# Performance work log

Hardware: AMD Instinct MI355X
Metric: run time of the kernel (lower is better)

Reference implementation:

```python
import jax, jax.numpy as jnp
import numpy as np

R = 2        # pixel-shuffle upscale
CN = 32      # channel_nums
COL = 3      # colors
NM = 6       # module_nums (2 convs each -> 12 backbone convs)
QMAX_A = 255.0   # uint8 activation fake-quant range
QMAX_W = 127.0   # int8 (narrow) weight fake-quant range


def fq_act(x, s):
    # Brevitas Uint8ActPerTensorFloat fake-quant with STE
    v = x / s
    q = jnp.clip(jnp.round(v), 0.0, QMAX_A)
    return s * (v + jax.lax.stop_gradient(q - v))


def fq_w(w, s):
    # Int8WeightPerTensorFloat (symmetric, narrow range) fake-quant with STE
    v = w / s
    q = jnp.clip(jnp.round(v), -QMAX_W, QMAX_W)
    return s * (v + jax.lax.stop_gradient(q - v))


def conv3(x, w, b):
    y = jax.lax.conv_general_dilated(
        x, w, window_strides=(1, 1), padding=((1, 1), (1, 1)),
        dimension_numbers=("NCHW", "OIHW", "NCHW"))
    return y + b[None, :, None, None]


def qblock(x, w, b, sw, act_s):
    # QuantConv3X3: quant_in -> quant conv (+bias) -> QuantReLU (relu + quant)
    xq = fq_act(x, act_s)
    y = conv3(xq, fq_w(w, sw), b)
    y = jax.nn.relu(y)
    return fq_act(y, act_s)


def pixel_shuffle(x, r):
    B, C, H, W = x.shape
    c = C // (r * r)
    x = x.reshape(B, c, r, r, H, W)
    x = x.transpose(0, 1, 4, 2, 5, 3)   # B, c, H, r, W, r
    return x.reshape(B, c, H * r, W * r)


def _forward(x, head_w, head_b, head_sw, bb_w, bb_b, bb_sw, tr_w, tr_b, tr_sw, act_s):
    y0 = qblock(x, head_w, head_b, head_sw, act_s)

    def step(y, p):
        w, b, sw = p
        return qblock(y, w, b, sw, act_s), None

    y, _ = jax.lax.scan(step, y0, (bb_w, bb_b, bb_sw))
    y = qblock(y + y0, tr_w, tr_b, tr_sw, act_s)   # act_type='linear' still hits QuantReLU branch
    y = jnp.clip(y, 0.0, 255.0)
    return pixel_shuffle(y, R)


def setup_inputs() -> dict:
    key = jax.random.key(0)
    ks = jax.random.split(key, 4)
    B, H, W = 8, 256, 256
    x = jax.random.uniform(ks[0], (B, COL, H, W), dtype=jnp.float32) * 255.0
    head_w = jax.random.normal(ks[1], (CN, COL, 3, 3), dtype=jnp.float32) * 0.05
    head_b = jnp.zeros((CN,), jnp.float32)
    bb_w = jax.random.normal(ks[2], (2 * NM, CN, CN, 3, 3), dtype=jnp.float32) * 0.05
    bb_b = jnp.zeros((2 * NM, CN), jnp.float32)
    tr_w = jax.random.normal(ks[3], (COL * R * R, CN, 3, 3), dtype=jnp.float32) * 0.05
    tr_b = jnp.zeros((COL * R * R,), jnp.float32)
    head_sw = jnp.max(jnp.abs(head_w)) / QMAX_W
    bb_sw = jnp.max(jnp.abs(bb_w), axis=(1, 2, 3, 4)) / QMAX_W
    tr_sw = jnp.max(jnp.abs(tr_w)) / QMAX_W
    act_s = jnp.float32(1.0)
    return dict(x=x, head_w=head_w, head_b=head_b, head_sw=head_sw,
                bb_w=bb_w, bb_b=bb_b, bb_sw=bb_sw,
                tr_w=tr_w, tr_b=tr_b, tr_sw=tr_sw, act_s=act_s)


def reference(x, head_w, head_b, head_sw, bb_w, bb_b, bb_sw, tr_w, tr_b, tr_sw, act_s):
    return _forward(x, head_w, head_b, head_sw, bb_w, bb_b, bb_sw, tr_w, tr_b, tr_sw, act_s)
```

## Files before the change

### kernel.cpp

```cpp
#include <hip/hip_runtime.h>

typedef __bf16 bf16x8 __attribute__((ext_vector_type(8)));
typedef float  f32x16 __attribute__((ext_vector_type(16)));

__global__ __launch_bounds__(256) void quantw_kernel(
    const float* __restrict__ src, float* __restrict__ dst,
    const float* __restrict__ sw, int per_layer_sw, int OC, int ICK, int total)
{
    int i = blockIdx.x * 256 + threadIdx.x;
    if (i >= total) return;
    int per = OC * ICK;
    int l = i / per;
    int rem = i - l * per;
    int oc = rem / ICK;
    int k = rem - oc * ICK;
    float s = sw[per_layer_sw ? l : 0];
    float v = rintf(src[i] / s);
    v = fminf(fmaxf(v, -127.0f), 127.0f);
    dst[l * per + k * OC + oc] = v;
}

__global__ __launch_bounds__(256) void packb_kernel(
    const float* __restrict__ src, unsigned short* __restrict__ dst,
    const float* __restrict__ sw, int per_layer_sw, int OC_real, int total)
{
    int i = blockIdx.x * 256 + threadIdx.x;
    if (i >= total) return;
    int l   = i / 9216;
    int r   = i - l * 9216;
    int s   = r >> 9;
    int lane = (r >> 3) & 63;
    int j   = r & 7;
    int k   = s * 16 + ((lane >> 5) << 3) + j;
    int tap = k >> 5;
    int ic  = k & 31;
    int oc  = lane & 31;
    unsigned short v = 0;
    if (oc < OC_real) {
        float scale = sw[per_layer_sw ? l : 0];
        float w = src[((l * OC_real + oc) * 32 + ic) * 9 + tap];
        float q = rintf(w / scale);
        q = fminf(fmaxf(q, -127.0f), 127.0f);
        union { float f; unsigned int u; } cv; cv.f = q;
        v = (unsigned short)(cv.u >> 16);
    }
    dst[i] = v;
}

__global__ __launch_bounds__(256) void head_kernel(
    const float* __restrict__ x, const float* __restrict__ wq,
    const float* __restrict__ bias, const float* __restrict__ sw_ptr,
    const float* __restrict__ s_ptr, unsigned char* __restrict__ out)
{
    __shared__ unsigned char tile[3][10][34];
    const int tid = threadIdx.x;
    const int x0 = blockIdx.x * 32;
    const int y0 = blockIdx.y * 8;
    const int b  = blockIdx.z;
    const float s = s_ptr[0];

    for (int ch = 0; ch < 3; ++ch) {
        const int base = (b * 3 + ch) << 16;
        for (int p = tid; p < 10 * 34; p += 256) {
            int r = p / 34, c = p - r * 34;
            int gy = y0 + r - 1, gx = x0 + c - 1;
            unsigned char v = 0;
            if ((unsigned)gy < 256u && (unsigned)gx < 256u) {
                float xv = x[base + (gy << 8) + gx];
                float q = (s == 1.0f) ? xv : (xv / s);
                q = rintf(q);
                q = fminf(fmaxf(q, 0.0f), 255.0f);
                v = (unsigned char)q;
            }
            tile[ch][r][c] = v;
        }
    }
    __syncthreads();

    const int c = tid & 31, r = tid >> 5;
    float acc[32];
    #pragma unroll
    for (int i = 0; i < 32; ++i) acc[i] = 0.0f;

    #pragma unroll
    for (int ic = 0; ic < 3; ++ic) {
        float a[9];
        #pragma unroll
        for (int dy = 0; dy < 3; ++dy)
            #pragma unroll
            for (int dx = 0; dx < 3; ++dx)
                a[dy * 3 + dx] = (float)tile[ic][r + dy][c + dx];
        #pragma unroll
        for (int t = 0; t < 9; ++t) {
            const float* wrow = wq + (ic * 9 + t) * 32;
            #pragma unroll
            for (int oc = 0; oc < 32; ++oc)
                acc[oc] = fmaf(a[t], wrow[oc], acc[oc]);
        }
    }

    const float alpha = s * sw_ptr[0];
    unsigned int w8[8] = {0,0,0,0,0,0,0,0};
    #pragma unroll
    for (int oc = 0; oc < 32; ++oc) {
        float y = fmaf(alpha, acc[oc], bias[oc]);
        y = fmaxf(y, 0.0f);
        float v = (s == 1.0f) ? y : (y / s);
        v = rintf(v);
        v = fminf(fmaxf(v, 0.0f), 255.0f);
        w8[oc >> 2] |= ((unsigned int)(unsigned char)v) << (8 * (oc & 3));
    }
    uint4* dst = (uint4*)(out + (size_t)((((b << 8) + (y0 + r)) << 8) + (x0 + c)) * 32);
    dst[0] = make_uint4(w8[0], w8[1], w8[2], w8[3]);
    dst[1] = make_uint4(w8[4], w8[5], w8[6], w8[7]);
}

template<bool FINAL>
__global__ __launch_bounds__(256, 2) void qconv_mfma_kernel(
    const unsigned char* __restrict__ in,
    const unsigned char* __restrict__ resid,
    const unsigned short* __restrict__ Bp,
    const float* __restrict__ bias,
    const float* __restrict__ sw_ptr, int sw_idx,
    const float* __restrict__ s_ptr,
    void* __restrict__ out)
{
    __shared__ uint4 aT[2448];
    __shared__ uint4 bT[1152];
    const int tid = threadIdx.x;
    const int x0 = blockIdx.x << 5;
    const int y0 = blockIdx.y << 4;
    const int b  = blockIdx.z;

    #pragma unroll
    for (int it = 0; it < 5; ++it) {
        int bi = tid + it * 256;
        if (bi < 1152) bT[bi] = ((const uint4*)Bp)[bi];
    }
    #pragma unroll
    for (int it = 0; it < 5; ++it) {
        int ci = tid + it * 256;
        if (ci < 1224) {
            int yt  = ci / 68;
            int rem = ci - yt * 68;
            int xt  = rem >> 1;
            int ch  = rem & 1;
            int gy = y0 + yt - 1;
            int gx = x0 + xt - 1;
            uint4 raw = make_uint4(0, 0, 0, 0);
            uint4 res = make_uint4(0, 0, 0, 0);
            if ((unsigned)gy < 256u && (unsigned)gx < 256u) {
                size_t off = (size_t)((((b << 8) + gy) << 8) + gx) * 32 + (ch << 4);
                raw = *(const uint4*)(in + off);
                if (FINAL) res = *(const uint4*)(resid + off);
            }
            unsigned int ow[8];
            const unsigned int* rw = (const unsigned int*)&raw;
            const unsigned int* rr = (const unsigned int*)&res;
            #pragma unroll
            for (int w = 0; w < 4; ++w) {
                unsigned int v = rw[w], rv = rr[w];
                #pragma unroll
                for (int hb = 0; hb < 2; ++hb) {
                    unsigned int a0 = (v >> (16 * hb)) & 0xffu;
                    unsigned int a1 = (v >> (16 * hb + 8)) & 0xffu;
                    if (FINAL) {
                        a0 += (rv >> (16 * hb)) & 0xffu;      if (a0 > 255u) a0 = 255u;
                        a1 += (rv >> (16 * hb + 8)) & 0xffu;  if (a1 > 255u) a1 = 255u;
                    }
                    union { float f; unsigned int u; } c0, c1;
                    c0.f = (float)a0; c1.f = (float)a1;
                    ow[2 * w + hb] = (c0.u >> 16) | (c1.u & 0xffff0000u);
                }
            }
            int swz  = (xt & 3) ^ ((xt >> 2) & 3);
            int base = (yt * 34 + xt) << 2;
            aT[base + (((ch << 1) + 0) ^ swz)] = make_uint4(ow[0], ow[1], ow[2], ow[3]);
            aT[base + (((ch << 1) + 1) ^ swz)] = make_uint4(ow[4], ow[5], ow[6], ow[7]);
        }
    }
    __syncthreads();

    const int lane = tid & 63;
    const int wid  = tid >> 6;
    const int px   = lane & 31;
    const int half = lane >> 5;
    const int py0  = wid << 2;

    f32x16 acc[4];
    #pragma unroll
    for (int p = 0; p < 4; ++p)
        #pragma unroll
        for (int i = 0; i < 16; ++i) acc[p][i] = 0.0f;

    #pragma unroll
    for (int ich = 0; ich < 2; ++ich) {
        bf16x8 af[6][3];
        #pragma unroll
        for (int yl = 0; yl < 6; ++yl) {
            #pragma unroll
            for (int dx = 0; dx < 3; ++dx) {
                int xt = px + dx;
                int cb = (ich << 1) + half;
                int chunk = ((py0 + yl) * 34 + xt) * 4 + (cb ^ ((xt & 3) ^ ((xt >> 2) & 3)));
                af[yl][dx] = *(const bf16x8*)&aT[chunk];
            }
        }
        #pragma unroll
        for (int t = 0; t < 9; ++t) {
            const int dy = t / 3, dx = t - dy * 3;
            bf16x8 wfr = *(const bf16x8*)&bT[((t << 1) + ich) * 64 + lane];
            acc[0] = __builtin_amdgcn_mfma_f32_32x32x16_bf16(wfr, af[dy + 0][dx], acc[0], 0, 0, 0);
            acc[1] = __builtin_amdgcn_mfma_f32_32x32x16_bf16(wfr, af[dy + 1][dx], acc[1], 0, 0, 0);
            acc[2] = __builtin_amdgcn_mfma_f32_32x32x16_bf16(wfr, af[dy + 2][dx], acc[2], 0, 0, 0);
            acc[3] = __builtin_amdgcn_mfma_f32_32x32x16_bf16(wfr, af[dy + 3][dx], acc[3], 0, 0, 0);
        }
    }

    const float s = s_ptr[0];
    const float alpha = s * sw_ptr[sw_idx];
    const int gx = x0 + px;

    if (!FINAL) {
        float bv[16];
        #pragma unroll
        for (int r = 0; r < 16; ++r)
            bv[r] = bias[(r & 3) + ((r >> 2) << 3) + (half << 2)];
        #pragma unroll
        for (int py = 0; py < 4; ++py) {
            const int gy = y0 + py0 + py;
            unsigned char* pout = (unsigned char*)out + (((size_t)((((b << 8) + gy) << 8) + gx)) << 5);
            #pragma unroll
            for (int q = 0; q < 4; ++q) {
                unsigned int wv = 0;
                #pragma unroll
                for (int j = 0; j < 4; ++j) {
                    float y = fmaf(alpha, acc[py][4 * q + j], bv[4 * q + j]);
                    y = fmaxf(y, 0.0f);
                    float v = (s == 1.0f) ? y : (y / s);
                    v = rintf(v);
                    v = fminf(fmaxf(v, 0.0f), 255.0f);
                    wv |= ((unsigned int)v) << (8 * j);
                }
                *(unsigned int*)(pout + 8 * q + 4 * half) = wv;
            }
        }
    } else {
        #pragma unroll
        for (int py = 0; py < 4; ++py) {
            const int gy = y0 + py0 + py;
            #pragma unroll
            for (int r = 0; r < 16; ++r) {
                const int oc = (r & 3) + ((r >> 2) << 3) + (half << 2);
                if (oc < 12) {
                    float y = fmaf(alpha, acc[py][r], bias[oc]);
                    y = fmaxf(y, 0.0f);
                    float v = (s == 1.0f) ? y : (y / s);
                    v = rintf(v);
                    v = fminf(fmaxf(v, 0.0f), 255.0f);
                    float o = (s == 1.0f) ? v : fminf(fmaxf(s * v, 0.0f), 255.0f);
                    const int cc = oc >> 2, r1 = (oc >> 1) & 1, r2 = oc & 1;
                    ((float*)out)[(size_t)(((b * 3 + cc) << 9) + (gy << 1) + r1) * 512 + (gx << 1) + r2] = o;
                }
            }
        }
    }
}

extern "C" void kernel_launch(void* const* d_in, const int* in_sizes, int n_in,
                              void* d_out, int out_size, void* d_ws, size_t ws_size,
                              hipStream_t stream) {
    const float* x       = (const float*)d_in[0];
    const float* head_w  = (const float*)d_in[1];
    const float* head_b  = (const float*)d_in[2];
    const float* head_sw = (const float*)d_in[3];
    const float* bb_w    = (const float*)d_in[4];
    const float* bb_b    = (const float*)d_in[5];
    const float* bb_sw   = (const float*)d_in[6];
    const float* tr_w    = (const float*)d_in[7];
    const float* tr_b    = (const float*)d_in[8];
    const float* tr_sw   = (const float*)d_in[9];
    const float* act_s   = (const float*)d_in[10];

    char* ws = (char*)d_ws;
    unsigned char* buf0 = (unsigned char*)ws;
    unsigned char* buf1 = buf0 + 16777216;
    unsigned char* buf2 = buf1 + 16777216;
    float* wqH = (float*)(ws + 50331648);
    unsigned short* BpB = (unsigned short*)(ws + 50331648 + 4096);
    unsigned short* BpT = BpB + 110592;

    quantw_kernel<<<(864 + 255) / 256, 256, 0, stream>>>(head_w, wqH, head_sw, 0, 32, 27, 864);
    packb_kernel<<<(110592 + 255) / 256, 256, 0, stream>>>(bb_w, BpB, bb_sw, 1, 32, 110592);
    packb_kernel<<<(9216 + 255) / 256, 256, 0, stream>>>(tr_w, BpT, tr_sw, 0, 12, 9216);

    head_kernel<<<dim3(8, 32, 8), 256, 0, stream>>>(x, wqH, head_b, head_sw, act_s, buf0);

    dim3 gridB(8, 16, 8);
    const unsigned char* cur = buf0;
    unsigned char* nxt = buf1;
    for (int l = 0; l < 12; ++l) {
        qconv_mfma_kernel<false><<<gridB, 256, 0, stream>>>(
            cur, nullptr, BpB + l * 9216, bb_b + l * 32, bb_sw, l, act_s, (void*)nxt);
        cur = nxt;
        nxt = (nxt == buf1) ? buf2 : buf1;
    }

    qconv_mfma_kernel<true><<<gridB, 256, 0, stream>>>(
        cur, buf0, BpT, tr_b, tr_sw, 0, act_s, d_out);
}
```

Baseline: 378.6 us.

## Drop weight LDS staging, read weights from global, restructure loop for occupancy

Removes the shared-memory copy of the packed weights and has each wave read its weight fragments straight from global memory (they should stay cached in L1/L2). The A-fragment loads are regrouped per dx, so only 6 fragments are live at a time instead of 18, and launch bounds rise to 4 blocks per CU. The goal is to cut LDS usage and register pressure so more blocks can be resident at once. In exchange, weight loads now hit the global/cache path inside the MFMA loop, and the tighter register limit could cause spills.

```diff
diff --git a/kernel.cpp b/kernel.cpp
--- a/kernel.cpp
+++ b/kernel.cpp
@@ -116,7 +116,7 @@
 }
 
 template<bool FINAL>
-__global__ __launch_bounds__(256, 2) void qconv_mfma_kernel(
+__global__ __launch_bounds__(256, 4) void qconv_mfma_kernel(
     const unsigned char* __restrict__ in,
     const unsigned char* __restrict__ resid,
     const unsigned short* __restrict__ Bp,
@@ -126,17 +126,11 @@
     void* __restrict__ out)
 {
     __shared__ uint4 aT[2448];
-    __shared__ uint4 bT[1152];
     const int tid = threadIdx.x;
     const int x0 = blockIdx.x << 5;
     const int y0 = blockIdx.y << 4;
     const int b  = blockIdx.z;
 
-    #pragma unroll
-    for (int it = 0; it < 5; ++it) {
-        int bi = tid + it * 256;
-        if (bi < 1152) bT[bi] = ((const uint4*)Bp)[bi];
-    }
     #pragma unroll
     for (int it = 0; it < 5; ++it) {
         int ci = tid + it * 256;
@@ -187,6 +181,8 @@
     const int half = lane >> 5;
     const int py0  = wid << 2;
 
+    const bf16x8* Wg = (const bf16x8*)Bp;
+
     f32x16 acc[4];
     #pragma unroll
     for (int p = 0; p < 4; ++p)
@@ -195,25 +191,23 @@
 
     #pragma unroll
     for (int ich = 0; ich < 2; ++ich) {
-        bf16x8 af[6][3];
-        #pragma unroll
-        for (int yl = 0; yl < 6; ++yl) {
-            #pragma unroll
-            for (int dx = 0; dx < 3; ++dx) {
-                int xt = px + dx;
-                int cb = (ich << 1) + half;
-                int chunk = ((py0 + yl) * 34 + xt) * 4 + (cb ^ ((xt & 3) ^ ((xt >> 2) & 3)));
-                af[yl][dx] = *(const bf16x8*)&aT[chunk];
-            }
-        }
-        #pragma unroll
-        for (int t = 0; t < 9; ++t) {
-            const int dy = t / 3, dx = t - dy * 3;
-            bf16x8 wfr = *(const bf16x8*)&bT[((t << 1) + ich) * 64 + lane];
-            acc[0] = __builtin_amdgcn_mfma_f32_32x32x16_bf16(wfr, af[dy + 0][dx], acc[0], 0, 0, 0);
-            acc[1] = __builtin_amdgcn_mfma_f32_32x32x16_bf16(wfr, af[dy + 1][dx], acc[1], 0, 0, 0);
-            acc[2] = __builtin_amdgcn_mfma_f32_32x32x16_bf16(wfr, af[dy + 2][dx], acc[2], 0, 0, 0);
-            acc[3] = __builtin_amdgcn_mfma_f32_32x32x16_bf16(wfr, af[dy + 3][dx], acc[3], 0, 0, 0);
+        const int cb = (ich << 1) + half;
+        #pragma unroll
+        for (int dx = 0; dx < 3; ++dx) {
+            const int xt = px + dx;
+            const int cbs = cb ^ ((xt & 3) ^ ((xt >> 2) & 3));
+            bf16x8 af[6];
+            #pragma unroll
+            for (int yl = 0; yl < 6; ++yl)
+                af[yl] = *(const bf16x8*)&aT[((py0 + yl) * 34 + xt) * 4 + cbs];
+            #pragma unroll
+            for (int dy = 0; dy < 3; ++dy) {
+                bf16x8 wfr = Wg[(((dy * 3 + dx) << 1) + ich) * 64 + lane];
+                acc[0] = __builtin_amdgcn_mfma_f32_32x32x16_bf16(wfr, af[dy + 0], acc[0], 0, 0, 0);
+                acc[1] = __builtin_amdgcn_mfma_f32_32x32x16_bf16(wfr, af[dy + 1], acc[1], 0, 0, 0);
+                acc[2] = __builtin_amdgcn_mfma_f32_32x32x16_bf16(wfr, af[dy + 2], acc[2], 0, 0, 0);
+                acc[3] = __builtin_amdgcn_mfma_f32_32x32x16_bf16(wfr, af[dy + 3], acc[3], 0, 0, 0);
+            }
         }
     }
 
```

Measured after the change: 349.5 us. 1.08x faster.
